# Optimization experiments

Measured on AMD Instinct MI355X. Metric: run time of the kernel, lower is better.

## Reference

```python
import jax, jax.numpy as jnp
import numpy as np
from jax import lax

VOCAB = 28996  # bert-base-cased vocab size (static for segment_sum)
B, S, D = 32, 512, 768
NUM_CLASSES = 9


def _lstm_dir(x, w_ih, w_hh, b_ih, b_hh):
    # x: [T, N, In]; torch gate order i, f, g, o packed along dim 0 of weights
    T, N, _ = x.shape
    H = w_hh.shape[1]
    xg = jnp.einsum('tni,gi->tng', x, w_ih) + b_ih  # precompute input projections [T,N,4H]

    def step(carry, xg_t):
        h, c = carry
        g = xg_t + h @ w_hh.T + b_hh
        i, f, gg, o = jnp.split(g, 4, axis=-1)
        c = jax.nn.sigmoid(f) * c + jax.nn.sigmoid(i) * jnp.tanh(gg)
        h = jax.nn.sigmoid(o) * jnp.tanh(c)
        return (h, c), h

    h0 = jnp.zeros((N, H), x.dtype)
    _, ys = lax.scan(step, (h0, h0), xg)
    return ys  # [T, N, H]


def setup_inputs() -> dict:
    key = jax.random.key(0)
    ks = jax.random.split(key, 8)
    H, In = D, 2 * D
    w = 0.02
    return {
        'batch': jax.random.randint(ks[0], (B, S), 0, VOCAB),
        'hidden': jax.random.normal(ks[1], (B, S, D), jnp.float32),
        'w_ih_f': jax.random.normal(ks[2], (4 * H, In), jnp.float32) * w,
        'w_hh_f': jax.random.normal(ks[3], (4 * H, H), jnp.float32) * w,
        'b_ih_f': jnp.zeros((4 * H,), jnp.float32),
        'b_hh_f': jnp.zeros((4 * H,), jnp.float32),
        'w_ih_b': jax.random.normal(ks[4], (4 * H, In), jnp.float32) * w,
        'w_hh_b': jax.random.normal(ks[5], (4 * H, H), jnp.float32) * w,
        'b_ih_b': jnp.zeros((4 * H,), jnp.float32),
        'b_hh_b': jnp.zeros((4 * H,), jnp.float32),
        'lin_w': jax.random.normal(ks[6], (NUM_CLASSES, 2 * H), jnp.float32) * w,
        'lin_b': jnp.zeros((NUM_CLASSES,), jnp.float32),
    }


def reference(batch, hidden, w_ih_f, w_hh_f, b_ih_f, b_hh_f,
              w_ih_b, w_hh_b, b_ih_b, b_hh_b, lin_w, lin_b):
    b, s, d = hidden.shape
    flat_ids = batch.reshape(-1)            # [B*S]
    flat_h = hidden.reshape(-1, d)          # [B*S, D]
    # segment mean of embeddings grouped by raw token id (the dict loop in torch)
    sums = jax.ops.segment_sum(flat_h, flat_ids, num_segments=VOCAB)
    counts = jax.ops.segment_sum(jnp.ones((flat_ids.shape[0], 1), hidden.dtype),
                                 flat_ids, num_segments=VOCAB)
    means = sums / jnp.maximum(counts, 1.0)
    ctx = means[flat_ids].reshape(b, s, d)  # gather-broadcast back per position
    x = jnp.concatenate([hidden, ctx], axis=2)  # [B, S, 2D]
    # nn.LSTM is not batch_first: scans over dim0 (B acts as time, S as batch)
    out_f = _lstm_dir(x, w_ih_f, w_hh_f, b_ih_f, b_hh_f)
    out_b = _lstm_dir(x[::-1], w_ih_b, w_hh_b, b_ih_b, b_hh_b)[::-1]
    out = jnp.concatenate([out_f, out_b], axis=-1)  # [B, S, 2D]
    # dropout is identity in eval mode
    return out @ lin_w.T + lin_b  # [B, S, num_classes]
```

## Files before the change

kernel.cpp:

```cpp
#include <hip/hip_runtime.h>

#define VOCAB 28996
#define BB 32
#define SS 512
#define DD 768
#define NCLS 9
#define ROWS (BB*SS)
#define IN2 (2*DD)
#define G4 (4*DD)
#define NB2 (2*G4)

typedef __attribute__((ext_vector_type(8))) short short8;
typedef __attribute__((ext_vector_type(4))) short shortx4;
typedef __attribute__((ext_vector_type(4))) float floatx4;
typedef unsigned long long ull;

__device__ __forceinline__ float bf2f(unsigned short u){
  union { unsigned int i; float f; } v; v.i = ((unsigned int)u) << 16; return v.f;
}
__device__ __forceinline__ unsigned short f2bf(float f){
  union { float f; unsigned int i; } v; v.f = f;
  unsigned int r = v.i + 0x7FFFu + ((v.i >> 16) & 1u);
  return (unsigned short)(r >> 16);
}
__device__ __forceinline__ float sigf(float x){ return 1.0f / (1.0f + __expf(-x)); }
__device__ __forceinline__ float tanhfast(float x){
  float y = fminf(fmaxf(x, -15.f), 15.f);
  float e = __expf(2.f * y);
  return 1.f - 2.f / (e + 1.f);
}

__device__ __forceinline__ void gl_lds16(const unsigned short* g, unsigned short* l){
  __builtin_amdgcn_global_load_lds((__attribute__((address_space(1))) void*)(g),
                                   (__attribute__((address_space(3))) void*)(l), 16, 0, 0);
}
__device__ __forceinline__ void gl_lds16_c(const unsigned short* g, unsigned short* l){
  __builtin_amdgcn_global_load_lds((__attribute__((address_space(1))) void*)(g),
                                   (__attribute__((address_space(3))) void*)(l), 16, 0, 17);
}
__device__ __forceinline__ void store16_sc1(unsigned short* p, short8 v){
  asm volatile("global_store_dwordx4 %0, %1, off sc0 sc1" :: "v"(p), "v"(v) : "memory");
}

#define VMCNT(n) do { asm volatile("s_waitcnt vmcnt(" #n ")" ::: "memory"); \
                      __builtin_amdgcn_sched_barrier(0); } while (0)

__global__ void seg_scatter(const int* __restrict__ ids, const float* __restrict__ hidden,
                            float* __restrict__ sums, float* __restrict__ counts)
{
  int r = blockIdx.x;
  int id = ids[r];
  const float* h = hidden + (long)r * DD;
  float* s = sums + (long)id * DD;
  for (int d = threadIdx.x; d < DD; d += 256)
    atomicAdd(&s[d], h[d]);
  if (threadIdx.x == 0) atomicAdd(&counts[id], 1.0f);
}

__global__ void build_x(const int* __restrict__ ids, const float* __restrict__ hidden,
                        const float* __restrict__ sums, const float* __restrict__ counts,
                        unsigned short* __restrict__ x)
{
  int r = blockIdx.x;
  int id = ids[r];
  float inv = 1.0f / fmaxf(counts[id], 1.0f);
  const float* h = hidden + (long)r * DD;
  const float* s = sums + (long)id * DD;
  unsigned short* xr = x + (long)r * IN2;
  for (int d = threadIdx.x; d < DD; d += 256) {
    xr[d]      = f2bf(h[d]);
    xr[DD + d] = f2bf(s[d] * inv);
  }
}

__global__ void conv_w_perm(const float* __restrict__ w, unsigned short* __restrict__ o, int K)
{
  long i = (long)blockIdx.x * 256 + threadIdx.x;
  if (i >= (long)G4 * K) return;
  int row = (int)(i / K); int k = (int)(i - (long)row * K);
  int u = row >> 2, g = row & 3;
  o[i] = f2bf(w[((long)(g * DD + u)) * K + k]);
}

__global__ void conv_bias_perm(const float* __restrict__ bif, const float* __restrict__ bhf,
                               const float* __restrict__ bib, const float* __restrict__ bhb,
                               float* __restrict__ o)
{
  int n = blockIdx.x * 256 + threadIdx.x;
  if (n >= NB2) return;
  int d = n / G4, rr = n - d * G4, u = rr >> 2, g = rr & 3;
  int s = g * DD + u;
  o[n] = d ? (bib[s] + bhb[s]) : (bif[s] + bhf[s]);
}

__global__ __launch_bounds__(256, 2)
void gemm_bt(const unsigned short* __restrict__ A, int lda,
             const unsigned short* __restrict__ B, int ldb,
             unsigned short* __restrict__ C, int ldc,
             const float* __restrict__ bias, int K)
{
  __shared__ unsigned short lA[128 * 32];
  __shared__ unsigned short lB[128 * 32];
  const int t = threadIdx.x;
  const int lane = t & 63;
  const int wv = t >> 6;
  const int wm = wv >> 1, wn = wv & 1;
  const int l15 = lane & 15, q = lane >> 4;
  const long m0 = (long)blockIdx.y * 128;
  const long n0 = (long)blockIdx.x * 128;
  const int rowS = t >> 2;
  const int kc = (((t & 3) ^ ((t >> 3) & 3))) * 8;
  const int qsw = (q ^ ((l15 >> 1) & 3)) * 8;
  const unsigned short* gA = A + (m0 + rowS) * lda + kc;
  const unsigned short* gB = B + (n0 + rowS) * ldb + kc;
  unsigned short* dA0 = lA + (wv << 9);
  unsigned short* dA1 = lA + 2048 + (wv << 9);
  unsigned short* dB0 = lB + (wv << 9);
  unsigned short* dB1 = lB + 2048 + (wv << 9);

  floatx4 acc[4][4];
  #pragma unroll
  for (int i = 0; i < 4; i++)
    #pragma unroll
    for (int j = 0; j < 4; j++)
      acc[i][j] = (floatx4){0.f, 0.f, 0.f, 0.f};

  const long a64 = (long)64 * lda;
  const long b64 = (long)64 * ldb;
  for (int kt = 0; kt < K; kt += 32) {
    gl_lds16(gA + kt,       dA0);
    gl_lds16(gA + a64 + kt, dA1);
    gl_lds16(gB + kt,       dB0);
    gl_lds16(gB + b64 + kt, dB1);
    __syncthreads();
    short8 af[4], bfr[4];
    #pragma unroll
    for (int i = 0; i < 4; i++)
      af[i] = *(const short8*)(lA + (wm * 64 + i * 16 + l15) * 32 + qsw);
    #pragma unroll
    for (int j = 0; j < 4; j++)
      bfr[j] = *(const short8*)(lB + (wn * 64 + j * 16 + l15) * 32 + qsw);
    #pragma unroll
    for (int i = 0; i < 4; i++)
      #pragma unroll
      for (int j = 0; j < 4; j++)
        acc[i][j] = __builtin_amdgcn_mfma_f32_16x16x32_bf16(af[i], bfr[j], acc[i][j], 0, 0, 0);
    __syncthreads();
  }

  #pragma unroll
  for (int i = 0; i < 4; i++) {
    #pragma unroll
    for (int j = 0; j < 4; j++) {
      const long mg = m0 + wm * 64 + i * 16 + q * 4;
      const long ng = n0 + wn * 64 + j * 16 + l15;
      const float bb = bias[ng];
      #pragma unroll
      for (int r = 0; r < 4; r++)
        C[(mg + r) * ldc + ng] = f2bf(acc[i][j][r] + bb);
    }
  }
}

__global__ __launch_bounds__(512, 1)
void lstm_persist(const unsigned short* __restrict__ xg, int ldxg,
                  const unsigned short* __restrict__ whh,
                  unsigned short* __restrict__ hbuf,
                  unsigned short* __restrict__ outc,
                  unsigned* bar,
                  int dir0, int ndir)
{
  __shared__ unsigned short bufA[2][16384];
  __shared__ unsigned short bufB[2][16384];
  __shared__ unsigned short hout[128 * 40];

  const int bid = blockIdx.x;
  const int xcd = bid & 7;
  const int idx = bid >> 3;
  int dm, k3;
  if (ndir == 2) { dm = idx & 7; k3 = idx >> 3; }
  else           { dm = idx & 3; k3 = idx >> 2; }
  const int ld  = (ndir == 2) ? (dm & 1) : 0;
  const int dir = dir0 + ld;
  const int mt  = (ndir == 2) ? (dm >> 1) : dm;
  const int nt  = k3 * 8 + xcd;
  const int m0 = mt * 128, n0 = nt * 128;
  const int u0 = n0 >> 2;
  unsigned* gbar = bar + dm * 16;
  const int nb24 = 24;

  const int t0 = threadIdx.x;
  const int lane = t0 & 63;
  const int wv = t0 >> 6;
  const int wm = wv >> 1;
  const int wn = wv & 1;
  const int l15 = lane & 15, q = lane >> 4;
  const long ldoff = (ndir == 2 && ld == 1) ? (long)G4 : 0;

  const unsigned short* Bdir = whh + (long)dir * G4 * DD;
  const int srow  = lane >> 2;
  const int scolA = (((lane & 3) ^ ((lane >> 3) & 3))) * 8;
  const int qsw   = (q ^ ((l15 >> 1) & 3)) * 8;

  const int rb = wv * 16 + srow;
  const unsigned short* wB  = Bdir + (long)(n0 + rb) * DD + scolA;
  const unsigned short* hA0 = hbuf + ((long)0 * ndir + ld) * ((long)SS * DD) + (long)(m0 + rb) * DD + scolA;
  const unsigned short* hA1 = hbuf + ((long)1 * ndir + ld) * ((long)SS * DD) + (long)(m0 + rb) * DD + scolA;

  float c_reg[2][4];
  #pragma unroll
  for (int i = 0; i < 2; i++)
    #pragma unroll
    for (int j = 0; j < 4; j++)
      c_reg[i][j] = 0.f;

  for (int s = 0; s < BB; s++) {
    const int tt = dir ? (BB - 1 - s) : s;
    const unsigned short* hA = (s & 1) ? hA1 : hA0;
    unsigned short* hw = hbuf + (((long)((s + 1) & 1)) * ndir + ld) * ((long)SS * DD);

    #pragma unroll
    for (int p = 0; p < 4; p++) {
      gl_lds16_c(hA + p * 32, &bufA[0][p * 4096 + wv * 512 + lane * 8]);
      gl_lds16 (wB + p * 32, &bufB[0][p * 4096 + wv * 512 + lane * 8]);
    }
    shortx4 xr0[4], xr1[4];
    {
      const unsigned short* xb = xg + ((long)tt * SS + m0) * ldxg + ldoff + n0;
      const unsigned short* xb0 = xb + (long)(wm * 32 + l15) * ldxg + wn * 64 + q * 4;
      const unsigned short* xb1 = xb0 + (long)16 * ldxg;
      #pragma unroll
      for (int j = 0; j < 4; j++) {
        xr0[j] = *(const shortx4*)(xb0 + j * 16);
        xr1[j] = *(const shortx4*)(xb1 + j * 16);
      }
    }

    floatx4 acc[2][4];
    #pragma unroll
    for (int i = 0; i < 2; i++)
      #pragma unroll
      for (int j = 0; j < 4; j++)
        acc[i][j] = (floatx4){0.f, 0.f, 0.f, 0.f};

    #pragma unroll
    for (int j6 = 0; j6 < 6; j6++) {
      if (j6 < 5) {
        const int b = (j6 + 1) & 1;
        const long kb = (long)(j6 + 1) * 128;
        #pragma unroll
        for (int p = 0; p < 4; p++) {
          gl_lds16_c(hA + kb + p * 32, &bufA[b][p * 4096 + wv * 512 + lane * 8]);
          gl_lds16 (wB + kb + p * 32, &bufB[b][p * 4096 + wv * 512 + lane * 8]);
        }
      }
      if (j6 == 0)      VMCNT(16);
      else if (j6 < 5)  VMCNT(8);
      else              VMCNT(0);
      __builtin_amdgcn_s_barrier();
      const int b = j6 & 1;
      __builtin_amdgcn_s_setprio(1);
      #pragma unroll
      for (int ks = 0; ks < 4; ks++) {
        const unsigned short* pA = &bufA[b][ks * 4096];
        const unsigned short* pB = &bufB[b][ks * 4096];
        short8 af[2], bfr[4];
        #pragma unroll
        for (int i = 0; i < 2; i++)
          af[i] = *(const short8*)(pA + (wm * 32 + i * 16 + l15) * 32 + qsw);
        #pragma unroll
        for (int j = 0; j < 4; j++)
          bfr[j] = *(const short8*)(pB + (wn * 64 + j * 16 + l15) * 32 + qsw);
        #pragma unroll
        for (int i = 0; i < 2; i++)
          #pragma unroll
          for (int j = 0; j < 4; j++)
            acc[i][j] = __builtin_amdgcn_mfma_f32_16x16x32_bf16(bfr[j], af[i], acc[i][j], 0, 0, 0);
      }
      __builtin_amdgcn_s_setprio(0);
      if (j6 < 5) __builtin_amdgcn_s_barrier();
    }

    #pragma unroll
    for (int i = 0; i < 2; i++) {
      const int mrow = wm * 32 + i * 16 + l15;
      #pragma unroll
      for (int j = 0; j < 4; j++) {
        const int nb = wn * 64 + j * 16 + q * 4;
        shortx4 xv = i ? xr1[j] : xr0[j];
        float gi = acc[i][j][0] + bf2f((unsigned short)xv[0]);
        float gf = acc[i][j][1] + bf2f((unsigned short)xv[1]);
        float gg = acc[i][j][2] + bf2f((unsigned short)xv[2]);
        float go = acc[i][j][3] + bf2f((unsigned short)xv[3]);
        float c = sigf(gf) * c_reg[i][j] + sigf(gi) * tanhfast(gg);
        float h = sigf(go) * tanhfast(c);
        c_reg[i][j] = c;
        hout[mrow * 40 + (nb >> 2)] = f2bf(h);
      }
    }
    __syncthreads();
    {
      const int row = t0 >> 2;
      const int qq = t0 & 3;
      short8 v0 = *(const short8*)(hout + row * 40 + qq * 8);
      unsigned short* hwp = hw + (long)(m0 + row) * DD + u0 + qq * 8;
      unsigned short* op  = outc + ((long)tt * SS + m0 + row) * IN2 + dir * DD + u0 + qq * 8;
      store16_sc1(hwp, v0);
      *(short8*)op = v0;
    }
    if (s < BB - 1) {
      VMCNT(0);
      __builtin_amdgcn_s_barrier();
      if (threadIdx.x == 0) {
        unsigned g = __hip_atomic_load(gbar + 1, __ATOMIC_RELAXED, __HIP_MEMORY_SCOPE_AGENT);
        unsigned a = __hip_atomic_fetch_add(gbar, 1u, __ATOMIC_RELAXED, __HIP_MEMORY_SCOPE_AGENT);
        if (a == (unsigned)(nb24 - 1)) {
          __hip_atomic_store(gbar, 0u, __ATOMIC_RELAXED, __HIP_MEMORY_SCOPE_AGENT);
          __hip_atomic_store(gbar + 1, g + 1u, __ATOMIC_RELEASE, __HIP_MEMORY_SCOPE_AGENT);
        } else {
          unsigned curv;
          do {
            __builtin_amdgcn_s_sleep(2);
            curv = __hip_atomic_load(gbar + 1, __ATOMIC_RELAXED, __HIP_MEMORY_SCOPE_AGENT);
          } while (curv == g);
        }
      }
      __builtin_amdgcn_s_barrier();
    }
  }
}

__global__ void final_linear(const unsigned short* __restrict__ xin, const float* __restrict__ w,
                             const float* __restrict__ b, float* __restrict__ out)
{
  __shared__ float red[NCLS * 256];
  int row = blockIdx.x;
  const unsigned short* x = xin + (long)row * IN2;
  float p[NCLS];
  #pragma unroll
  for (int c = 0; c < NCLS; c++) p[c] = 0.f;
  for (int k = threadIdx.x; k < IN2; k += 256) {
    float xv = bf2f(x[k]);
    #pragma unroll
    for (int c = 0; c < NCLS; c++) p[c] += xv * w[c * IN2 + k];
  }
  #pragma unroll
  for (int c = 0; c < NCLS; c++) red[c * 256 + threadIdx.x] = p[c];
  __syncthreads();
  for (int s = 128; s > 0; s >>= 1) {
    if (threadIdx.x < s) {
      #pragma unroll
      for (int c = 0; c < NCLS; c++)
        red[c * 256 + threadIdx.x] += red[c * 256 + threadIdx.x + s];
    }
    __syncthreads();
  }
  if (threadIdx.x < NCLS)
    out[(long)row * NCLS + threadIdx.x] = red[threadIdx.x * 256] + b[threadIdx.x];
}

extern "C" void kernel_launch(void* const* d_in, const int* in_sizes, int n_in,
                              void* d_out, int out_size, void* d_ws, size_t ws_size,
                              hipStream_t stream)
{
  const int*   batch  = (const int*)d_in[0];
  const float* hidden = (const float*)d_in[1];
  const float* w_ih_f = (const float*)d_in[2];
  const float* w_hh_f = (const float*)d_in[3];
  const float* b_ih_f = (const float*)d_in[4];
  const float* b_hh_f = (const float*)d_in[5];
  const float* w_ih_b = (const float*)d_in[6];
  const float* w_hh_b = (const float*)d_in[7];
  const float* b_ih_b = (const float*)d_in[8];
  const float* b_hh_b = (const float*)d_in[9];
  const float* lin_w  = (const float*)d_in[10];
  const float* lin_b  = (const float*)d_in[11];
  float* out = (float*)d_out;

  char* ws = (char*)d_ws;
  size_t off = 0;
  auto alloc = [&](size_t bytes) -> char* {
    char* p = ws + off;
    off += (bytes + 255) & ~(size_t)255;
    return p;
  };

  const size_t SZ_XG_A = (size_t)ROWS * NB2 * 2;
  const size_t SZ_XG_B = (size_t)ROWS * G4  * 2;
  const size_t SZ_XBF  = (size_t)ROWS * IN2 * 2;
  const size_t SZ_W    = (size_t)G4 * IN2 * 2;
  const size_t SZ_BIAS = (size_t)NB2 * 4;
  const size_t SZ_HBUF = (size_t)2 * 2 * SS * DD * 2;
  const size_t SZ_BAR  = 512;
  const size_t SZ_SUMS = (size_t)VOCAB * DD * 4 + (size_t)VOCAB * 4;

  const size_t NEED_C = SZ_XG_A + SZ_XBF + SZ_W + SZ_BIAS + SZ_HBUF + SZ_BAR + 8 * 256;
  const bool combined = ws_size >= NEED_C;

  const long nWIH = (long)G4 * IN2;
  const long nWHH = (long)G4 * DD;

  if (combined) {
    unsigned short* xg   = (unsigned short*)alloc(SZ_XG_A);
    unsigned short* xbf  = (unsigned short*)alloc(SZ_XBF);
    unsigned short* wbuf = (unsigned short*)alloc(SZ_W);
    float*          bias = (float*)alloc(SZ_BIAS);
    unsigned short* hbuf = (unsigned short*)alloc(SZ_HBUF);
    unsigned*       bar  = (unsigned*)alloc(SZ_BAR);
    float* sums   = (float*)xg;
    float* counts = sums + (size_t)VOCAB * DD;

    hipMemsetAsync(sums, 0, SZ_SUMS, stream);
    hipMemsetAsync(bar, 0, SZ_BAR, stream);
    seg_scatter<<<ROWS, 256, 0, stream>>>(batch, hidden, sums, counts);
    build_x<<<ROWS, 256, 0, stream>>>(batch, hidden, sums, counts, xbf);
    conv_bias_perm<<<(NB2 + 255) / 256, 256, 0, stream>>>(b_ih_f, b_hh_f, b_ih_b, b_hh_b, bias);

    for (int dir = 0; dir < 2; dir++) {
      conv_w_perm<<<(unsigned)((nWIH + 255) / 256), 256, 0, stream>>>(dir ? w_ih_b : w_ih_f, wbuf, IN2);
      dim3 grid(G4 / 128, ROWS / 128, 1);
      gemm_bt<<<grid, 256, 0, stream>>>(xbf, IN2, wbuf, IN2,
                                        xg + (size_t)dir * G4, NB2,
                                        bias + (size_t)dir * G4, IN2);
    }
    conv_w_perm<<<(unsigned)((nWHH + 255) / 256), 256, 0, stream>>>(w_hh_f, wbuf, DD);
    conv_w_perm<<<(unsigned)((nWHH + 255) / 256), 256, 0, stream>>>(w_hh_b, wbuf + (size_t)G4 * DD, DD);

    hipMemsetAsync(hbuf, 0, SZ_HBUF, stream);
    lstm_persist<<<192, 512, 0, stream>>>(xg, NB2, wbuf, hbuf, xbf, bar, 0, 2);
    final_linear<<<ROWS, 256, 0, stream>>>(xbf, lin_w, lin_b, out);
  } else {
    unsigned short* xg   = (unsigned short*)alloc(SZ_XG_B);
    unsigned short* xbf  = (unsigned short*)alloc(SZ_XBF);
    unsigned short* outc = (unsigned short*)alloc(SZ_XBF);
    unsigned short* wih  = (unsigned short*)alloc(SZ_W);
    unsigned short* whh  = (unsigned short*)alloc(SZ_W);
    float*          bias = (float*)alloc(SZ_BIAS);
    unsigned short* hbuf = (unsigned short*)alloc(SZ_HBUF);
    unsigned*       bar  = (unsigned*)alloc(SZ_BAR);
    float* sums   = (float*)xg;
    float* counts = sums + (size_t)VOCAB * DD;

    hipMemsetAsync(sums, 0, SZ_SUMS, stream);
    hipMemsetAsync(bar, 0, SZ_BAR, stream);
    seg_scatter<<<ROWS, 256, 0, stream>>>(batch, hidden, sums, counts);
    build_x<<<ROWS, 256, 0, stream>>>(batch, hidden, sums, counts, xbf);
    conv_bias_perm<<<(NB2 + 255) / 256, 256, 0, stream>>>(b_ih_f, b_hh_f, b_ih_b, b_hh_b, bias);
    conv_w_perm<<<(unsigned)((nWHH + 255) / 256), 256, 0, stream>>>(w_hh_f, whh, DD);
    conv_w_perm<<<(unsigned)((nWHH + 255) / 256), 256, 0, stream>>>(w_hh_b, whh + (size_t)G4 * DD, DD);

    for (int dir = 0; dir < 2; dir++) {
      conv_w_perm<<<(unsigned)((nWIH + 255) / 256), 256, 0, stream>>>(dir ? w_ih_b : w_ih_f, wih, IN2);
      {
        dim3 grid(G4 / 128, ROWS / 128, 1);
        gemm_bt<<<grid, 256, 0, stream>>>(xbf, IN2, wih, IN2, xg, G4,
                                          bias + (size_t)dir * G4, IN2);
      }
      hipMemsetAsync(hbuf, 0, SZ_HBUF, stream);
      lstm_persist<<<96, 512, 0, stream>>>(xg, G4, whh, hbuf, outc, bar, dir, 1);
    }
    final_linear<<<ROWS, 256, 0, stream>>>(outc, lin_w, lin_b, out);
  }
}
```

Before: 1.235 ms.

## Replace input-projection GEMM with 256x256 double-buffered pipelined tile kernel

Swaps the 128x128 single-buffered bf16 GEMM used for the LSTM input projections for a 256x256 tile kernel with 512 threads. It double-buffers 64-wide K slices in LDS and prefetches the next slice in pieces between MFMA groups, using vmcnt waits and raw barriers plus setprio around the MFMA bursts. The goal is more reuse per load and hiding global-to-LDS latency behind compute. In exchange it uses much more LDS and registers, runs one block per CU, and hardcodes 24 K iterations, so it only works for K=1536.

```diff
diff --git a/kernel.cpp b/kernel.cpp
--- a/kernel.cpp
+++ b/kernel.cpp
@@ -93,71 +93,104 @@
   o[n] = d ? (bib[s] + bhb[s]) : (bif[s] + bhf[s]);
 }
 
-__global__ __launch_bounds__(256, 2)
-void gemm_bt(const unsigned short* __restrict__ A, int lda,
-             const unsigned short* __restrict__ B, int ldb,
-             unsigned short* __restrict__ C, int ldc,
-             const float* __restrict__ bias, int K)
-{
-  __shared__ unsigned short lA[128 * 32];
-  __shared__ unsigned short lB[128 * 32];
+__global__ __launch_bounds__(512, 1)
+void gemm_bt256(const unsigned short* __restrict__ A, int lda,
+                const unsigned short* __restrict__ B, int ldb,
+                unsigned short* __restrict__ C, int ldc,
+                const float* __restrict__ bias, int K)
+{
+  __shared__ unsigned short lA[2][16384];
+  __shared__ unsigned short lB[2][16384];
   const int t = threadIdx.x;
   const int lane = t & 63;
   const int wv = t >> 6;
-  const int wm = wv >> 1, wn = wv & 1;
+  const int wm = wv >> 1;
+  const int wn = wv & 1;
   const int l15 = lane & 15, q = lane >> 4;
-  const long m0 = (long)blockIdx.y * 128;
-  const long n0 = (long)blockIdx.x * 128;
-  const int rowS = t >> 2;
-  const int kc = (((t & 3) ^ ((t >> 3) & 3))) * 8;
+  const long m0 = (long)blockIdx.x * 256;
+  const long n0 = (long)blockIdx.y * 256;
+  const int rs  = t >> 2;
+  const int sc  = (((t & 3) ^ ((t >> 3) & 3))) * 8;
   const int qsw = (q ^ ((l15 >> 1) & 3)) * 8;
-  const unsigned short* gA = A + (m0 + rowS) * lda + kc;
-  const unsigned short* gB = B + (n0 + rowS) * ldb + kc;
-  unsigned short* dA0 = lA + (wv << 9);
-  unsigned short* dA1 = lA + 2048 + (wv << 9);
-  unsigned short* dB0 = lB + (wv << 9);
-  unsigned short* dB1 = lB + 2048 + (wv << 9);
-
-  floatx4 acc[4][4];
+
+  const unsigned short* gA = A + (m0 + rs) * (long)lda + sc;
+  const unsigned short* gB = B + (n0 + rs) * (long)ldb + sc;
+  const long a128 = (long)128 * lda;
+  const long b128 = (long)128 * ldb;
+
+  #define PIECE(b, kt, p, hf) do {                                               \
+    const long kb_ = (long)(kt) * 64 + (p) * 32 + (hf) * 0;                      \
+    gl_lds16(gA + kb_ + (hf) * a128, &lA[b][(p) * 8192 + (hf) * 4096 + t * 8]);  \
+    gl_lds16(gB + kb_ + (hf) * b128, &lB[b][(p) * 8192 + (hf) * 4096 + t * 8]);  \
+  } while (0)
+
+  floatx4 acc[4][8];
   #pragma unroll
   for (int i = 0; i < 4; i++)
     #pragma unroll
-    for (int j = 0; j < 4; j++)
+    for (int j = 0; j < 8; j++)
       acc[i][j] = (floatx4){0.f, 0.f, 0.f, 0.f};
 
-  const long a64 = (long)64 * lda;
-  const long b64 = (long)64 * ldb;
-  for (int kt = 0; kt < K; kt += 32) {
-    gl_lds16(gA + kt,       dA0);
-    gl_lds16(gA + a64 + kt, dA1);
-    gl_lds16(gB + kt,       dB0);
-    gl_lds16(gB + b64 + kt, dB1);
-    __syncthreads();
-    short8 af[4], bfr[4];
-    #pragma unroll
-    for (int i = 0; i < 4; i++)
-      af[i] = *(const short8*)(lA + (wm * 64 + i * 16 + l15) * 32 + qsw);
-    #pragma unroll
-    for (int j = 0; j < 4; j++)
-      bfr[j] = *(const short8*)(lB + (wn * 64 + j * 16 + l15) * 32 + qsw);
-    #pragma unroll
-    for (int i = 0; i < 4; i++)
-      #pragma unroll
-      for (int j = 0; j < 4; j++)
-        acc[i][j] = __builtin_amdgcn_mfma_f32_16x16x32_bf16(af[i], bfr[j], acc[i][j], 0, 0, 0);
-    __syncthreads();
-  }
+  PIECE(0, 0, 0, 0); PIECE(0, 0, 0, 1);
+  PIECE(0, 0, 1, 0); PIECE(0, 0, 1, 1);
+
+  #pragma unroll 2
+  for (int kt = 0; kt < 24; kt++) {
+    const int cur = kt & 1;
+    const int nxt = cur ^ 1;
+    const unsigned short* pA = &lA[cur][0];
+    const unsigned short* pB = &lB[cur][0];
+
+    VMCNT(4);
+    __builtin_amdgcn_s_barrier();
+
+    #pragma unroll
+    for (int ks = 0; ks < 2; ks++) {
+      short8 bfr[8];
+      #pragma unroll
+      for (int ih = 0; ih < 2; ih++) {
+        if (kt < 23) {
+          if (ks == 0 && ih == 0) PIECE(nxt, kt + 1, 0, 0);
+          if (ks == 0 && ih == 1) PIECE(nxt, kt + 1, 0, 1);
+          if (ks == 1 && ih == 0) PIECE(nxt, kt + 1, 1, 0);
+          if (ks == 1 && ih == 1) PIECE(nxt, kt + 1, 1, 1);
+        }
+        if (ih == 0) {
+          #pragma unroll
+          for (int j = 0; j < 8; j++)
+            bfr[j] = *(const short8*)(pB + ks * 8192 + (wn * 128 + j * 16 + l15) * 32 + qsw);
+        }
+        short8 af[2];
+        #pragma unroll
+        for (int ii = 0; ii < 2; ii++)
+          af[ii] = *(const short8*)(pA + ks * 8192 + (wm * 64 + (ih * 2 + ii) * 16 + l15) * 32 + qsw);
+        __builtin_amdgcn_s_setprio(1);
+        #pragma unroll
+        for (int ii = 0; ii < 2; ii++)
+          #pragma unroll
+          for (int j = 0; j < 8; j++)
+            acc[ih * 2 + ii][j] =
+              __builtin_amdgcn_mfma_f32_16x16x32_bf16(af[ii], bfr[j], acc[ih * 2 + ii][j], 0, 0, 0);
+        __builtin_amdgcn_s_setprio(0);
+      }
+      if (ks == 0) {
+        if (kt < 23) VMCNT(4); else VMCNT(0);
+        __builtin_amdgcn_s_barrier();
+      }
+    }
+  }
+  #undef PIECE
 
   #pragma unroll
   for (int i = 0; i < 4; i++) {
     #pragma unroll
-    for (int j = 0; j < 4; j++) {
+    for (int j = 0; j < 8; j++) {
       const long mg = m0 + wm * 64 + i * 16 + q * 4;
-      const long ng = n0 + wn * 64 + j * 16 + l15;
+      const long ng = n0 + wn * 128 + j * 16 + l15;
       const float bb = bias[ng];
       #pragma unroll
       for (int r = 0; r < 4; r++)
-        C[(mg + r) * ldc + ng] = f2bf(acc[i][j][r] + bb);
+        C[(mg + r) * (long)ldc + ng] = f2bf(acc[i][j][r] + bb);
     }
   }
 }
@@ -418,10 +451,10 @@
 
     for (int dir = 0; dir < 2; dir++) {
       conv_w_perm<<<(unsigned)((nWIH + 255) / 256), 256, 0, stream>>>(dir ? w_ih_b : w_ih_f, wbuf, IN2);
-      dim3 grid(G4 / 128, ROWS / 128, 1);
-      gemm_bt<<<grid, 256, 0, stream>>>(xbf, IN2, wbuf, IN2,
-                                        xg + (size_t)dir * G4, NB2,
-                                        bias + (size_t)dir * G4, IN2);
+      dim3 grid(ROWS / 256, G4 / 256, 1);
+      gemm_bt256<<<grid, 512, 0, stream>>>(xbf, IN2, wbuf, IN2,
+                                           xg + (size_t)dir * G4, NB2,
+                                           bias + (size_t)dir * G4, IN2);
     }
     conv_w_perm<<<(unsigned)((nWHH + 255) / 256), 256, 0, stream>>>(w_hh_f, wbuf, DD);
     conv_w_perm<<<(unsigned)((nWHH + 255) / 256), 256, 0, stream>>>(w_hh_b, wbuf + (size_t)G4 * DD, DD);
@@ -452,9 +485,9 @@
     for (int dir = 0; dir < 2; dir++) {
       conv_w_perm<<<(unsigned)((nWIH + 255) / 256), 256, 0, stream>>>(dir ? w_ih_b : w_ih_f, wih, IN2);
       {
-        dim3 grid(G4 / 128, ROWS / 128, 1);
-        gemm_bt<<<grid, 256, 0, stream>>>(xbf, IN2, wih, IN2, xg, G4,
-                                          bias + (size_t)dir * G4, IN2);
+        dim3 grid(ROWS / 256, G4 / 256, 1);
+        gemm_bt256<<<grid, 512, 0, stream>>>(xbf, IN2, wih, IN2, xg, G4,
+                                             bias + (size_t)dir * G4, IN2);
       }
       hipMemsetAsync(hbuf, 0, SZ_HBUF, stream);
       lstm_persist<<<96, 512, 0, stream>>>(xg, G4, whh, hbuf, outc, bar, dir, 1);
```

Result: faster. 1.169 ms (-5.3%).
